# Performance work log

Measured on AMD Instinct MI355X. Metric: run time of the kernel, lower is better.

Reference implementation:

```python
import jax, jax.numpy as jnp
import numpy as np

N = 50000   # n_nodes (== input_dim, featureless identity features)
E = 800000  # edges per support (avg degree 16)
D = 200     # embed_dim (hardcoded in GIN)
C = 10      # num_classes


def setup_inputs() -> dict:
    key = jax.random.key(0)
    ks = jax.random.split(key, 8)
    x = jnp.zeros((N, 1), jnp.float32)  # unused: layer 0 is featureless
    rows0 = jax.random.randint(ks[0], (E,), 0, N, dtype=jnp.int32)
    cols0 = jax.random.randint(ks[1], (E,), 0, N, dtype=jnp.int32)
    vals0 = jax.random.uniform(ks[2], (E,), jnp.float32)
    rows1 = jax.random.randint(ks[3], (E,), 0, N, dtype=jnp.int32)
    cols1 = jax.random.randint(ks[4], (E,), 0, N, dtype=jnp.int32)
    vals1 = jax.random.uniform(ks[5], (E,), jnp.float32)
    W0 = jax.random.normal(ks[6], (N, D), jnp.float32) * 0.02
    W1 = jax.random.normal(ks[7], (D, C), jnp.float32) * 0.05
    eps0 = jnp.zeros((1,), jnp.float32)  # train_eps init (~1e-4 in repo)
    eps1 = jnp.zeros((1,), jnp.float32)
    return dict(x=x, rows0=rows0, cols0=cols0, vals0=vals0,
                rows1=rows1, cols1=cols1, vals1=vals1,
                W0=W0, W1=W1, eps0=eps0, eps1=eps1)


def reference(x, rows0, cols0, vals0, rows1, cols1, vals1, W0, W1, eps0, eps1):
    # sparse A @ X via gather + segment-sum (A in COO: rows, cols, vals)
    def spmm(r, c, v, X):
        return jax.ops.segment_sum(v[:, None] * X[c], r, num_segments=N)

    # Layer 0 (featureless, num_mlp_layers==1):
    #   AX = sum_i A_i ; out = AX @ W0 + 0.1*(1+eps0)*W0
    h0 = spmm(rows0, cols0, vals0, W0) + spmm(rows1, cols1, vals1, W0) \
         + 0.1 * (1.0 + eps0[0]) * W0
    h = jax.nn.relu(h0)  # [N, D]

    # Layer 1 (with features): out = (sum_i A_i @ h + 0.1*(1+eps1)*h) @ W1
    ax = spmm(rows0, cols0, vals0, h) + spmm(rows1, cols1, vals1, h)
    out = (ax + 0.1 * (1.0 + eps1[0]) * h) @ W1  # [N, C]
    return out
```

## Files before the change

kernel.cpp:

```cpp
#include <hip/hip_runtime.h>

#define N_NODES 50000
#define E_EDGES 800000
#define E2      (2 * E_EDGES)
#define D_DIM   200
#define C_CLS   10
#define NB_BUCKET ((N_NODES + 255) / 256)
#define BATCH     4096
#define CAP       12288
#define SENT      0xFFFFu

static __device__ __forceinline__ unsigned short f2bf(float f) {
    unsigned u = __float_as_uint(f);
    return (unsigned short)((u + 0x7FFFu + ((u >> 16) & 1u)) >> 16);
}
static __device__ __forceinline__ float bf_lo(unsigned u) {
    return __uint_as_float(u << 16);
}
static __device__ __forceinline__ float bf_hi(unsigned u) {
    return __uint_as_float(u & 0xFFFF0000u);
}

__global__ __launch_bounds__(256) void convert_w0_kernel(const float* __restrict__ W0,
                                                         unsigned short* __restrict__ W0h,
                                                         int* __restrict__ bcur) {
    if (blockIdx.x == 0 && threadIdx.x < NB_BUCKET) bcur[threadIdx.x] = 0;
    int i = (blockIdx.x * 256 + threadIdx.x) * 4;
    if (i >= N_NODES * D_DIM) return;
    float4 f = *(const float4*)(W0 + i);
    uint2 p;
    p.x = (unsigned)f2bf(f.x) | ((unsigned)f2bf(f.y) << 16);
    p.y = (unsigned)f2bf(f.z) | ((unsigned)f2bf(f.w) << 16);
    *(uint2*)(W0h + i) = p;
}

__global__ __launch_bounds__(256) void bucket_scatter_kernel(
        const int* __restrict__ rows0, const int* __restrict__ cols0,
        const float* __restrict__ vals0,
        const int* __restrict__ rows1, const int* __restrict__ cols1,
        const float* __restrict__ vals1,
        int* __restrict__ bcur,
        int2* __restrict__ stage) {
    __shared__ int cntL[NB_BUCKET];
    __shared__ int baseL[NB_BUCKET];
    __shared__ int offL[NB_BUCKET];
    __shared__ int2 recL[BATCH];
    const int tid = threadIdx.x;
    const int e0 = blockIdx.x * BATCH;

    for (int b = tid; b < NB_BUCKET; b += 256) cntL[b] = 0;
    __syncthreads();

#pragma unroll
    for (int k = 0; k < BATCH / 256; ++k) {
        int idx = k * 256 + tid;
        int e = e0 + idx;
        if (e < E2) {
            int r, c;
            float v;
            if (e < E_EDGES) {
                r = rows0[e]; c = cols0[e]; v = vals0[e];
            } else {
                int e1 = e - E_EDGES;
                r = rows1[e1]; c = cols1[e1]; v = vals1[e1];
            }
            recL[idx] = make_int2((int)((unsigned)r | ((unsigned)c << 16)),
                                  __float_as_int(v));
            atomicAdd(&cntL[r >> 8], 1);
        }
    }
    __syncthreads();

    for (int b = tid; b < NB_BUCKET; b += 256) {
        int c = cntL[b];
        int cpad = (c + 7) & ~7;
        int base = (cpad > 0) ? atomicAdd(&bcur[b], cpad) : 0;
        baseL[b] = base;
        offL[b] = 0;
        int2* bp = stage + (size_t)b * CAP;
        for (int s = base + c; s < base + cpad; ++s)
            bp[s] = make_int2((int)SENT, 0);
    }
    __syncthreads();

#pragma unroll
    for (int k = 0; k < BATCH / 256; ++k) {
        int idx = k * 256 + tid;
        int e = e0 + idx;
        if (e < E2) {
            int2 rec = recL[idx];
            int b = (int)(((unsigned)rec.x & 0xFFFFu) >> 8);
            int pos = baseL[b] + atomicAdd(&offL[b], 1);
            stage[(size_t)b * CAP + pos] = rec;
        }
    }
}

__global__ __launch_bounds__(256) void hist_scan_kernel(const int* __restrict__ bcur,
                                                        const int2* __restrict__ stage,
                                                        int* __restrict__ excl,
                                                        int* __restrict__ bsum) {
    __shared__ int hist[256];
    __shared__ int ws4[4];
    const int b = blockIdx.x;
    const int tid = threadIdx.x;
    const int lane = tid & 63;
    const int w = tid >> 6;
    hist[tid] = 0;
    __syncthreads();

    const int n = bcur[b];
    const int2* __restrict__ sp = stage + (size_t)b * CAP;
    for (int i = tid; i < n; i += 256) {
        unsigned u = (unsigned)sp[i].x;
        if ((u & 0xFFFFu) != SENT)
            atomicAdd(&hist[u & 255u], 1);
    }
    __syncthreads();

    int v = hist[tid];
    int orig = v;
#pragma unroll
    for (int off = 1; off < 64; off <<= 1) {
        int t = __shfl_up(v, off, 64);
        if (lane >= off) v += t;
    }
    if (lane == 63) ws4[w] = v;
    __syncthreads();
    if (tid == 0) {
        int s = 0;
#pragma unroll
        for (int k = 0; k < 4; ++k) { int t = ws4[k]; ws4[k] = s; s += t; }
    }
    __syncthreads();
    v += ws4[w];

    const int row = (b << 8) + tid;
    if (row < N_NODES) excl[row] = v - orig;
    if (tid == 255) bsum[b] = v;
}

__global__ __launch_bounds__(64) void scan2_kernel(int* __restrict__ bsum,
                                                   int* __restrict__ row_ptr) {
    const int lane = threadIdx.x;
    int carry = 0;
    for (int base = 0; base < NB_BUCKET; base += 64) {
        int idx = base + lane;
        int v = (idx < NB_BUCKET) ? bsum[idx] : 0;
        int orig = v;
#pragma unroll
        for (int off = 1; off < 64; off <<= 1) {
            int t = __shfl_up(v, off, 64);
            if (lane >= off) v += t;
        }
        int chunk_total = __shfl(v, 63, 64);
        int ex = v - orig + carry;
        if (idx < NB_BUCKET) bsum[idx] = ex;
        carry += chunk_total;
    }
    if (lane == 0) row_ptr[N_NODES] = carry;
}

__global__ __launch_bounds__(256) void sort_place_kernel(const int* __restrict__ excl,
                                                         const int* __restrict__ bsum,
                                                         const int* __restrict__ bcur,
                                                         const int2* __restrict__ stage,
                                                         int* __restrict__ row_ptr,
                                                         unsigned* __restrict__ cv4) {
    __shared__ int lcur[256];
    const int b = blockIdx.x;
    const int tid = threadIdx.x;
    const int base = bsum[b];
    const int row = (b << 8) + tid;
    int ex = base + ((row < N_NODES) ? excl[row] : 0);
    if (row < N_NODES) row_ptr[row] = ex;
    lcur[tid] = ex;
    __syncthreads();

    const int n = bcur[b];
    const int2* __restrict__ sp = stage + (size_t)b * CAP;
    for (int i = tid; i < n; i += 256) {
        int2 rec = sp[i];
        unsigned u = (unsigned)rec.x;
        if ((u & 0xFFFFu) == SENT) continue;
        int pos = atomicAdd(&lcur[u & 255u], 1);
        cv4[pos] = (u & 0xFFFF0000u) | (unsigned)f2bf(__int_as_float(rec.y));
    }
}

__global__ __launch_bounds__(256) void spmm_layer0_fused_kernel(
        const int*  __restrict__ row_ptr,
        const unsigned* __restrict__ cv4,
        const unsigned short* __restrict__ W0h,
        const float* __restrict__ W1,
        const float* __restrict__ eps0,
        float* __restrict__ g) {
    __shared__ float W1s[D_DIM * C_CLS];
    for (int i = threadIdx.x; i < D_DIM * C_CLS; i += blockDim.x) W1s[i] = W1[i];
    __syncthreads();

    const int lane = threadIdx.x & 63;
    const int n = __builtin_amdgcn_readfirstlane(blockIdx.x * 4 + (threadIdx.x >> 6));
    if (n >= N_NODES) return;
    const float s0 = 0.1f * (1.0f + eps0[0]);
    const bool act = (lane < 50);
    const uint2* __restrict__ F = (const uint2*)W0h;

    const int beg  = row_ptr[n];
    const int endp = row_ptr[n + 1];
    float a0 = 0.f, a1 = 0.f, a2 = 0.f, a3 = 0.f;

    int e = beg;
    for (; e + 8 <= endp; e += 8) {
        unsigned w0 = cv4[e],     w1 = cv4[e + 1], w2 = cv4[e + 2], w3 = cv4[e + 3];
        unsigned w4 = cv4[e + 4], w5 = cv4[e + 5], w6 = cv4[e + 6], w7 = cv4[e + 7];
        if (act) {
            uint2 u0 = F[(size_t)(w0 >> 16) * 50 + lane];
            uint2 u1 = F[(size_t)(w1 >> 16) * 50 + lane];
            uint2 u2 = F[(size_t)(w2 >> 16) * 50 + lane];
            uint2 u3 = F[(size_t)(w3 >> 16) * 50 + lane];
            uint2 u4 = F[(size_t)(w4 >> 16) * 50 + lane];
            uint2 u5 = F[(size_t)(w5 >> 16) * 50 + lane];
            uint2 u6 = F[(size_t)(w6 >> 16) * 50 + lane];
            uint2 u7 = F[(size_t)(w7 >> 16) * 50 + lane];
            float v0 = __uint_as_float(w0 << 16), v1 = __uint_as_float(w1 << 16);
            float v2 = __uint_as_float(w2 << 16), v3 = __uint_as_float(w3 << 16);
            float v4 = __uint_as_float(w4 << 16), v5 = __uint_as_float(w5 << 16);
            float v6 = __uint_as_float(w6 << 16), v7 = __uint_as_float(w7 << 16);
            a0 += v0 * bf_lo(u0.x) + v1 * bf_lo(u1.x) + v2 * bf_lo(u2.x) + v3 * bf_lo(u3.x)
                + v4 * bf_lo(u4.x) + v5 * bf_lo(u5.x) + v6 * bf_lo(u6.x) + v7 * bf_lo(u7.x);
            a1 += v0 * bf_hi(u0.x) + v1 * bf_hi(u1.x) + v2 * bf_hi(u2.x) + v3 * bf_hi(u3.x)
                + v4 * bf_hi(u4.x) + v5 * bf_hi(u5.x) + v6 * bf_hi(u6.x) + v7 * bf_hi(u7.x);
            a2 += v0 * bf_lo(u0.y) + v1 * bf_lo(u1.y) + v2 * bf_lo(u2.y) + v3 * bf_lo(u3.y)
                + v4 * bf_lo(u4.y) + v5 * bf_lo(u5.y) + v6 * bf_lo(u6.y) + v7 * bf_lo(u7.y);
            a3 += v0 * bf_hi(u0.y) + v1 * bf_hi(u1.y) + v2 * bf_hi(u2.y) + v3 * bf_hi(u3.y)
                + v4 * bf_hi(u4.y) + v5 * bf_hi(u5.y) + v6 * bf_hi(u6.y) + v7 * bf_hi(u7.y);
        }
    }
    for (; e + 4 <= endp; e += 4) {
        unsigned w0 = cv4[e], w1 = cv4[e + 1], w2 = cv4[e + 2], w3 = cv4[e + 3];
        if (act) {
            uint2 u0 = F[(size_t)(w0 >> 16) * 50 + lane];
            uint2 u1 = F[(size_t)(w1 >> 16) * 50 + lane];
            uint2 u2 = F[(size_t)(w2 >> 16) * 50 + lane];
            uint2 u3 = F[(size_t)(w3 >> 16) * 50 + lane];
            float v0 = __uint_as_float(w0 << 16), v1 = __uint_as_float(w1 << 16);
            float v2 = __uint_as_float(w2 << 16), v3 = __uint_as_float(w3 << 16);
            a0 += v0 * bf_lo(u0.x) + v1 * bf_lo(u1.x) + v2 * bf_lo(u2.x) + v3 * bf_lo(u3.x);
            a1 += v0 * bf_hi(u0.x) + v1 * bf_hi(u1.x) + v2 * bf_hi(u2.x) + v3 * bf_hi(u3.x);
            a2 += v0 * bf_lo(u0.y) + v1 * bf_lo(u1.y) + v2 * bf_lo(u2.y) + v3 * bf_lo(u3.y);
            a3 += v0 * bf_hi(u0.y) + v1 * bf_hi(u1.y) + v2 * bf_hi(u2.y) + v3 * bf_hi(u3.y);
        }
    }
    for (; e < endp; ++e) {
        unsigned w = cv4[e];
        if (act) {
            uint2 u = F[(size_t)(w >> 16) * 50 + lane];
            float v = __uint_as_float(w << 16);
            a0 += v * bf_lo(u.x);
            a1 += v * bf_hi(u.x);
            a2 += v * bf_lo(u.y);
            a3 += v * bf_hi(u.y);
        }
    }

    float o[C_CLS];
#pragma unroll
    for (int k = 0; k < C_CLS; ++k) o[k] = 0.f;

    if (act) {
        uint2 w = F[(size_t)n * 50 + lane];
        a0 = fmaxf(a0 + s0 * bf_lo(w.x), 0.f);
        a1 = fmaxf(a1 + s0 * bf_hi(w.x), 0.f);
        a2 = fmaxf(a2 + s0 * bf_lo(w.y), 0.f);
        a3 = fmaxf(a3 + s0 * bf_hi(w.y), 0.f);
        const int d = lane * 4;
#pragma unroll
        for (int k = 0; k < C_CLS; ++k) {
            o[k] = a0 * W1s[(d + 0) * C_CLS + k]
                 + a1 * W1s[(d + 1) * C_CLS + k]
                 + a2 * W1s[(d + 2) * C_CLS + k]
                 + a3 * W1s[(d + 3) * C_CLS + k];
        }
    }

#pragma unroll
    for (int k = 0; k < C_CLS; ++k) {
        for (int off = 32; off > 0; off >>= 1)
            o[k] += __shfl_xor(o[k], off, 64);
    }

    if (lane == 0) {
        float* gp = g + (size_t)n * C_CLS;
#pragma unroll
        for (int k = 0; k < C_CLS; ++k) gp[k] = o[k];
    }
}

__global__ __launch_bounds__(256) void spmm_layer1_light_kernel(
        const int*  __restrict__ row_ptr,
        const unsigned* __restrict__ cv4,
        const float* __restrict__ g,
        const float* __restrict__ eps1,
        float* __restrict__ out) {
    const int lane = threadIdx.x & 63;
    const int n = __builtin_amdgcn_readfirstlane(blockIdx.x * 4 + (threadIdx.x >> 6));
    if (n >= N_NODES) return;
    const int grp = lane / 10;
    const int d   = lane - grp * 10;
    const float s1 = 0.1f * (1.0f + eps1[0]);

    const int beg  = row_ptr[n];
    const int endp = row_ptr[n + 1];
    float acc = 0.f;

    for (int base = beg; base < endp; base += 6) {
        int e = base + grp;
        if (grp < 6 && e < endp) {
            unsigned p = cv4[e];
            float vf = __uint_as_float(p << 16);
            acc += vf * g[(size_t)(p >> 16) * C_CLS + d];
        }
    }

    float t;
    t = __shfl(acc, lane + 10, 64); if (lane < 50) acc += t;
    t = __shfl(acc, lane + 20, 64); if (lane < 30) acc += t;
    t = __shfl(acc, lane + 40, 64); if (lane < 10) acc += t;

    if (lane < 10) {
        out[(size_t)n * C_CLS + d] = acc + s1 * g[(size_t)n * C_CLS + d];
    }
}

extern "C" void kernel_launch(void* const* d_in, const int* in_sizes, int n_in,
                              void* d_out, int out_size, void* d_ws, size_t ws_size,
                              hipStream_t stream) {
    const int*   rows0 = (const int*)d_in[1];
    const int*   cols0 = (const int*)d_in[2];
    const float* vals0 = (const float*)d_in[3];
    const int*   rows1 = (const int*)d_in[4];
    const int*   cols1 = (const int*)d_in[5];
    const float* vals1 = (const float*)d_in[6];
    const float* W0    = (const float*)d_in[7];
    const float* W1    = (const float*)d_in[8];
    const float* eps0  = (const float*)d_in[9];
    const float* eps1  = (const float*)d_in[10];
    float* out = (float*)d_out;

    char* ws = (char*)d_ws;
    size_t off = 0;
    auto alloc = [&](size_t bytes) {
        void* p = ws + off;
        off += (bytes + 255) & ~(size_t)255;
        return p;
    };
    unsigned short* W0h = (unsigned short*)alloc((size_t)N_NODES * D_DIM * 2);
    float* g      = (float*)alloc((size_t)N_NODES * C_CLS * 4);
    int* excl     = (int*)alloc((size_t)N_NODES * 4);
    int* bsum     = (int*)alloc((size_t)NB_BUCKET * 4);
    int* row_ptr  = (int*)alloc((size_t)(N_NODES + 1) * 4);
    int* bcur     = (int*)alloc((size_t)NB_BUCKET * 4);
    unsigned* cv4 = (unsigned*)alloc((size_t)E2 * 4);
    int2* stage   = (int2*)alloc((size_t)NB_BUCKET * CAP * 8);
    (void)ws_size;

    convert_w0_kernel<<<(N_NODES * D_DIM / 4 + 255) / 256, 256, 0, stream>>>(W0, W0h, bcur);
    bucket_scatter_kernel<<<(E2 + BATCH - 1) / BATCH, 256, 0, stream>>>(
        rows0, cols0, vals0, rows1, cols1, vals1, bcur, stage);
    hist_scan_kernel<<<NB_BUCKET, 256, 0, stream>>>(bcur, stage, excl, bsum);
    scan2_kernel<<<1, 64, 0, stream>>>(bsum, row_ptr);
    sort_place_kernel<<<NB_BUCKET, 256, 0, stream>>>(excl, bsum, bcur, stage, row_ptr, cv4);

    const int spmm_grid = (N_NODES + 3) / 4;
    spmm_layer0_fused_kernel<<<spmm_grid, 256, 0, stream>>>(
        row_ptr, cv4, W0h, W1, eps0, g);
    spmm_layer1_light_kernel<<<spmm_grid, 256, 0, stream>>>(
        row_ptr, cv4, g, eps1, out);
}
```

Before: 287.1 us.

## Fuse CSR build kernels, use atomic ticket offsets and per-row segments

Merges the W0 bf16 conversion into the bucket-scatter launch as extra blocks, and folds the histogram, two-level scan and placement kernels into one build_csr kernel. Bucket base offsets now come from an atomic ticket instead of a global scan, so each row stores a (start, count) segment rather than a prefix-sum row_ptr. Sentinel padding is dropped. The layer-1 SpMM loop is unrolled to two edges per group. This removes three launches and the serial scan, at the cost of a non-deterministic bucket order in cv4.

Measured after the change: 273.8 us. 4.6% less time.

```diff
diff --git a/kernel.cpp b/kernel.cpp
--- a/kernel.cpp
+++ b/kernel.cpp
@@ -5,14 +5,15 @@
 #define E2      (2 * E_EDGES)
 #define D_DIM   200
 #define C_CLS   10
-#define NB_BUCKET ((N_NODES + 255) / 256)
+#define NB_BUCKET 196
 #define BATCH     4096
+#define NB_SCATTER ((E2 + BATCH - 1) / BATCH)
+#define NB_CONV    ((N_NODES * D_DIM / 4 + 255) / 256)
 #define CAP       12288
-#define SENT      0xFFFFu
-
-static __device__ __forceinline__ unsigned short f2bf(float f) {
+
+static __device__ __forceinline__ unsigned f2bf(float f) {
     unsigned u = __float_as_uint(f);
-    return (unsigned short)((u + 0x7FFFu + ((u >> 16) & 1u)) >> 16);
+    return (u + 0x7FFFu + ((u >> 16) & 1u)) >> 16;
 }
 static __device__ __forceinline__ float bf_lo(unsigned u) {
     return __uint_as_float(u << 16);
@@ -21,20 +22,8 @@
     return __uint_as_float(u & 0xFFFF0000u);
 }
 
-__global__ __launch_bounds__(256) void convert_w0_kernel(const float* __restrict__ W0,
-                                                         unsigned short* __restrict__ W0h,
-                                                         int* __restrict__ bcur) {
-    if (blockIdx.x == 0 && threadIdx.x < NB_BUCKET) bcur[threadIdx.x] = 0;
-    int i = (blockIdx.x * 256 + threadIdx.x) * 4;
-    if (i >= N_NODES * D_DIM) return;
-    float4 f = *(const float4*)(W0 + i);
-    uint2 p;
-    p.x = (unsigned)f2bf(f.x) | ((unsigned)f2bf(f.y) << 16);
-    p.y = (unsigned)f2bf(f.z) | ((unsigned)f2bf(f.w) << 16);
-    *(uint2*)(W0h + i) = p;
-}
-
-__global__ __launch_bounds__(256) void bucket_scatter_kernel(
+__global__ __launch_bounds__(256) void convert_scatter_kernel(
+        const float* __restrict__ W0, unsigned short* __restrict__ W0h,
         const int* __restrict__ rows0, const int* __restrict__ cols0,
         const float* __restrict__ vals0,
         const int* __restrict__ rows1, const int* __restrict__ cols1,
@@ -45,6 +34,19 @@
     __shared__ int baseL[NB_BUCKET];
     __shared__ int offL[NB_BUCKET];
     __shared__ int2 recL[BATCH];
+
+    if (blockIdx.x >= NB_SCATTER) {
+        int i = ((blockIdx.x - NB_SCATTER) * 256 + threadIdx.x) * 4;
+        if (i < N_NODES * D_DIM) {
+            float4 f = *(const float4*)(W0 + i);
+            uint2 p;
+            p.x = f2bf(f.x) | (f2bf(f.y) << 16);
+            p.y = f2bf(f.z) | (f2bf(f.w) << 16);
+            *(uint2*)(W0h + i) = p;
+        }
+        return;
+    }
+
     const int tid = threadIdx.x;
     const int e0 = blockIdx.x * BATCH;
 
@@ -73,13 +75,8 @@
 
     for (int b = tid; b < NB_BUCKET; b += 256) {
         int c = cntL[b];
-        int cpad = (c + 7) & ~7;
-        int base = (cpad > 0) ? atomicAdd(&bcur[b], cpad) : 0;
-        baseL[b] = base;
+        baseL[b] = (c > 0) ? atomicAdd(&bcur[b], c) : 0;
         offL[b] = 0;
-        int2* bp = stage + (size_t)b * CAP;
-        for (int s = base + c; s < base + cpad; ++s)
-            bp[s] = make_int2((int)SENT, 0);
     }
     __syncthreads();
 
@@ -96,12 +93,16 @@
     }
 }
 
-__global__ __launch_bounds__(256) void hist_scan_kernel(const int* __restrict__ bcur,
-                                                        const int2* __restrict__ stage,
-                                                        int* __restrict__ excl,
-                                                        int* __restrict__ bsum) {
+__global__ __launch_bounds__(256) void build_csr_kernel(
+        const int* __restrict__ bcur,
+        const int2* __restrict__ stage,
+        int* __restrict__ ticket,
+        int2* __restrict__ rowseg,
+        unsigned* __restrict__ cv4) {
     __shared__ int hist[256];
+    __shared__ int lcur[256];
     __shared__ int ws4[4];
+    __shared__ int sbase;
     const int b = blockIdx.x;
     const int tid = threadIdx.x;
     const int lane = tid & 63;
@@ -111,15 +112,12 @@
 
     const int n = bcur[b];
     const int2* __restrict__ sp = stage + (size_t)b * CAP;
-    for (int i = tid; i < n; i += 256) {
-        unsigned u = (unsigned)sp[i].x;
-        if ((u & 0xFFFFu) != SENT)
-            atomicAdd(&hist[u & 255u], 1);
-    }
+    for (int i = tid; i < n; i += 256)
+        atomicAdd(&hist[(unsigned)sp[i].x & 255u], 1);
     __syncthreads();
 
     int v = hist[tid];
-    int orig = v;
+    const int orig = v;
 #pragma unroll
     for (int off = 1; off < 64; off <<= 1) {
         int t = __shfl_up(v, off, 64);
@@ -135,61 +133,25 @@
     __syncthreads();
     v += ws4[w];
 
+    if (tid == 255) sbase = atomicAdd(ticket, v);
+    __syncthreads();
+
+    const int start = sbase + v - orig;
     const int row = (b << 8) + tid;
-    if (row < N_NODES) excl[row] = v - orig;
-    if (tid == 255) bsum[b] = v;
-}
-
-__global__ __launch_bounds__(64) void scan2_kernel(int* __restrict__ bsum,
-                                                   int* __restrict__ row_ptr) {
-    const int lane = threadIdx.x;
-    int carry = 0;
-    for (int base = 0; base < NB_BUCKET; base += 64) {
-        int idx = base + lane;
-        int v = (idx < NB_BUCKET) ? bsum[idx] : 0;
-        int orig = v;
-#pragma unroll
-        for (int off = 1; off < 64; off <<= 1) {
-            int t = __shfl_up(v, off, 64);
-            if (lane >= off) v += t;
-        }
-        int chunk_total = __shfl(v, 63, 64);
-        int ex = v - orig + carry;
-        if (idx < NB_BUCKET) bsum[idx] = ex;
-        carry += chunk_total;
-    }
-    if (lane == 0) row_ptr[N_NODES] = carry;
-}
-
-__global__ __launch_bounds__(256) void sort_place_kernel(const int* __restrict__ excl,
-                                                         const int* __restrict__ bsum,
-                                                         const int* __restrict__ bcur,
-                                                         const int2* __restrict__ stage,
-                                                         int* __restrict__ row_ptr,
-                                                         unsigned* __restrict__ cv4) {
-    __shared__ int lcur[256];
-    const int b = blockIdx.x;
-    const int tid = threadIdx.x;
-    const int base = bsum[b];
-    const int row = (b << 8) + tid;
-    int ex = base + ((row < N_NODES) ? excl[row] : 0);
-    if (row < N_NODES) row_ptr[row] = ex;
-    lcur[tid] = ex;
-    __syncthreads();
-
-    const int n = bcur[b];
-    const int2* __restrict__ sp = stage + (size_t)b * CAP;
+    if (row < N_NODES) rowseg[row] = make_int2(start, orig);
+    lcur[tid] = start;
+    __syncthreads();
+
     for (int i = tid; i < n; i += 256) {
         int2 rec = sp[i];
         unsigned u = (unsigned)rec.x;
-        if ((u & 0xFFFFu) == SENT) continue;
         int pos = atomicAdd(&lcur[u & 255u], 1);
-        cv4[pos] = (u & 0xFFFF0000u) | (unsigned)f2bf(__int_as_float(rec.y));
+        cv4[pos] = (u & 0xFFFF0000u) | f2bf(__int_as_float(rec.y));
     }
 }
 
 __global__ __launch_bounds__(256) void spmm_layer0_fused_kernel(
-        const int*  __restrict__ row_ptr,
+        const int2* __restrict__ rowseg,
         const unsigned* __restrict__ cv4,
         const unsigned short* __restrict__ W0h,
         const float* __restrict__ W1,
@@ -206,8 +168,9 @@
     const bool act = (lane < 50);
     const uint2* __restrict__ F = (const uint2*)W0h;
 
-    const int beg  = row_ptr[n];
-    const int endp = row_ptr[n + 1];
+    const int2 seg = rowseg[n];
+    const int beg  = seg.x;
+    const int endp = seg.x + seg.y;
     float a0 = 0.f, a1 = 0.f, a2 = 0.f, a3 = 0.f;
 
     int e = beg;
@@ -298,7 +261,7 @@
 }
 
 __global__ __launch_bounds__(256) void spmm_layer1_light_kernel(
-        const int*  __restrict__ row_ptr,
+        const int2* __restrict__ rowseg,
         const unsigned* __restrict__ cv4,
         const float* __restrict__ g,
         const float* __restrict__ eps1,
@@ -310,16 +273,21 @@
     const int d   = lane - grp * 10;
     const float s1 = 0.1f * (1.0f + eps1[0]);
 
-    const int beg  = row_ptr[n];
-    const int endp = row_ptr[n + 1];
+    const int2 seg = rowseg[n];
+    const int beg  = seg.x;
+    const int endp = seg.x + seg.y;
     float acc = 0.f;
 
-    for (int base = beg; base < endp; base += 6) {
-        int e = base + grp;
-        if (grp < 6 && e < endp) {
-            unsigned p = cv4[e];
-            float vf = __uint_as_float(p << 16);
-            acc += vf * g[(size_t)(p >> 16) * C_CLS + d];
+    for (int base = beg; base < endp; base += 12) {
+        if (grp < 6) {
+            int ea = base + grp;
+            int eb = base + 6 + grp;
+            unsigned pa = (ea < endp) ? cv4[ea] : 0u;
+            unsigned pb = (eb < endp) ? cv4[eb] : 0u;
+            if (ea < endp)
+                acc += __uint_as_float(pa << 16) * g[(size_t)(pa >> 16) * C_CLS + d];
+            if (eb < endp)
+                acc += __uint_as_float(pb << 16) * g[(size_t)(pb >> 16) * C_CLS + d];
         }
     }
 
@@ -357,24 +325,21 @@
     };
     unsigned short* W0h = (unsigned short*)alloc((size_t)N_NODES * D_DIM * 2);
     float* g      = (float*)alloc((size_t)N_NODES * C_CLS * 4);
-    int* excl     = (int*)alloc((size_t)N_NODES * 4);
-    int* bsum     = (int*)alloc((size_t)NB_BUCKET * 4);
-    int* row_ptr  = (int*)alloc((size_t)(N_NODES + 1) * 4);
-    int* bcur     = (int*)alloc((size_t)NB_BUCKET * 4);
+    int2* rowseg  = (int2*)alloc((size_t)N_NODES * 8);
+    int* bcur     = (int*)alloc((size_t)(NB_BUCKET + 1) * 4);
     unsigned* cv4 = (unsigned*)alloc((size_t)E2 * 4);
     int2* stage   = (int2*)alloc((size_t)NB_BUCKET * CAP * 8);
+    int* ticket   = bcur + NB_BUCKET;
     (void)ws_size;
 
-    convert_w0_kernel<<<(N_NODES * D_DIM / 4 + 255) / 256, 256, 0, stream>>>(W0, W0h, bcur);
-    bucket_scatter_kernel<<<(E2 + BATCH - 1) / BATCH, 256, 0, stream>>>(
-        rows0, cols0, vals0, rows1, cols1, vals1, bcur, stage);
-    hist_scan_kernel<<<NB_BUCKET, 256, 0, stream>>>(bcur, stage, excl, bsum);
-    scan2_kernel<<<1, 64, 0, stream>>>(bsum, row_ptr);
-    sort_place_kernel<<<NB_BUCKET, 256, 0, stream>>>(excl, bsum, bcur, stage, row_ptr, cv4);
+    hipMemsetAsync(bcur, 0, (size_t)(NB_BUCKET + 1) * 4, stream);
+    convert_scatter_kernel<<<NB_SCATTER + NB_CONV, 256, 0, stream>>>(
+        W0, W0h, rows0, cols0, vals0, rows1, cols1, vals1, bcur, stage);
+    build_csr_kernel<<<NB_BUCKET, 256, 0, stream>>>(bcur, stage, ticket, rowseg, cv4);
 
     const int spmm_grid = (N_NODES + 3) / 4;
     spmm_layer0_fused_kernel<<<spmm_grid, 256, 0, stream>>>(
-        row_ptr, cv4, W0h, W1, eps0, g);
+        rowseg, cv4, W0h, W1, eps0, g);
     spmm_layer1_light_kernel<<<spmm_grid, 256, 0, stream>>>(
-        row_ptr, cv4, g, eps1, out);
-}
+        rowseg, cv4, g, eps1, out);
+}
```
